# Kernel tuning notes

Measured on AMD Instinct MI355X. Metric: run time of the kernel, lower is better.

The kernel has to match this reference:

```python
import jax, jax.numpy as jnp
import numpy as np

B, N, SK, D, H = 4, 1024, 1024, 1024, 16
HD = D // H  # head_dim = 64


def _ln(x, w, b):
    # torch LayerNorm: biased variance, eps=1e-6
    m = x.mean(-1, keepdims=True)
    v = x.var(-1, keepdims=True)
    return (x - m) * jax.lax.rsqrt(v + 1e-6) * w + b


def setup_inputs() -> dict:
    key = jax.random.key(0)
    ks = jax.random.split(key, 16)
    def w(k, shape, s=0.02):
        return jax.random.normal(k, shape, jnp.float32) * s
    return dict(
        x=jax.random.normal(ks[0], (B, N, D), jnp.float32),
        k=jax.random.normal(ks[1], (N, H, SK, HD), jnp.float32),
        v=jax.random.normal(ks[2], (N, H, SK, HD), jnp.float32),
        qkv_w=w(ks[3], (D, 3 * D)), qkv_b=w(ks[4], (3 * D,)),
        sa_proj_w=w(ks[5], (D, D)), sa_proj_b=w(ks[6], (D,)),
        q_w=w(ks[7], (D, D)), q_b=w(ks[8], (D,)),
        ed_proj_w=w(ks[9], (D, D)), ed_proj_b=w(ks[10], (D,)),
        fc1_w=w(ks[11], (D, 4 * D)), fc1_b=w(ks[12], (4 * D,)),
        fc2_w=w(ks[13], (4 * D, D)), fc2_b=w(ks[14], (D,)),
        ln1_w=jnp.ones((D,)), ln1_b=jnp.zeros((D,)),
        ln2_w=jnp.ones((D,)), ln2_b=jnp.zeros((D,)),
        ln3_w=jnp.ones((D,)), ln3_b=jnp.zeros((D,)),
    )


def reference(x, k, v, qkv_w, qkv_b, sa_proj_w, sa_proj_b, q_w, q_b,
              ed_proj_w, ed_proj_b, fc1_w, fc1_b, fc2_w, fc2_b,
              ln1_w, ln1_b, ln2_w, ln2_b, ln3_w, ln3_b):
    scale = HD ** -0.5
    # ---- SelfAttention (faithful to the original, unusual einsums) ----
    qkv = (x @ qkv_w + qkv_b).reshape(B, N, 3, H, HD).transpose(2, 1, 3, 0, 4)
    q_s, k_s, v_s = qkv[0], qkv[1], qkv[2]  # each [N, H, B, HD]
    # no shared contraction index between k and q -> outer product of reductions
    dp = jnp.einsum('kabc,qdef->qabe', k_s, q_s) * scale  # [N, H, B, B]
    sc = jax.nn.softmax(dp, axis=-1)  # attn_p = 0.0 -> dropout is identity
    wa = jnp.einsum('qabc,kdef->bqaf', sc, v_s).reshape(B, N, D)
    sa = wa @ sa_proj_w + sa_proj_b
    h1 = _ln(sa + x, ln1_w, ln1_b)
    # ---- EncoderDecoderAttention ----
    qc = (h1 @ q_w + q_b).reshape(B, N, H, HD).transpose(1, 2, 0, 3)  # [N, H, B, HD]
    dp2 = jnp.einsum('abkd,abqd->abqk', k, qc) * scale  # [N, H, B, SK]
    sc2 = jax.nn.softmax(dp2, axis=-1)
    wa2 = jnp.einsum('abts,abse->tabe', sc2, v).reshape(B, N, D)
    ca = wa2 @ ed_proj_w + ed_proj_b
    h2 = _ln(ca + x, ln2_w, ln2_b)  # residual uses x (as in source)
    # ---- MLP (exact GELU, p=0 dropout) ----
    z = jax.nn.gelu(h2 @ fc1_w + fc1_b, approximate=False) @ fc2_w + fc2_b
    return _ln(z + h2, ln3_w, ln3_b)
```

## Files before the change

kernel.cpp:

```cpp
#include <hip/hip_runtime.h>
#include <hip/hip_bf16.h>
#include <math.h>

typedef __attribute__((ext_vector_type(8))) short bf16x8;
typedef __attribute__((ext_vector_type(4))) float f32x4;

__device__ __forceinline__ void gll16(const void* g, const void* l) {
  __builtin_amdgcn_global_load_lds((__attribute__((address_space(1))) void*)g,
                                   (__attribute__((address_space(3))) void*)l, 16, 0, 0);
}

__device__ __forceinline__ unsigned short bf16bits(float f) {
  __hip_bfloat16 h = __float2bfloat16(f);
  return *reinterpret_cast<unsigned short*>(&h);
}

__global__ __launch_bounds__(256) void k_transpose_bf16(
    const float* __restrict__ W, __hip_bfloat16* __restrict__ WT, int R, int C)
{
  __shared__ float t[32][33];
  const int c0 = blockIdx.x << 5, r0 = blockIdx.y << 5;
  const int tx = threadIdx.x & 31, ty = threadIdx.x >> 5;
#pragma unroll
  for (int i = 0; i < 32; i += 8)
    t[ty + i][tx] = W[(size_t)(r0 + ty + i) * C + c0 + tx];
  __syncthreads();
#pragma unroll
  for (int i = 0; i < 32; i += 8)
    WT[(size_t)(c0 + ty + i) * R + r0 + tx] = __float2bfloat16(t[tx][ty + i]);
}

__global__ __launch_bounds__(256) void k_colsum_part(const float* __restrict__ x, float* __restrict__ part) {
  const int d = blockIdx.x * 256 + threadIdx.x;
  const int r0 = blockIdx.y * 128;
  float acc = 0.f;
  for (int r = 0; r < 128; ++r) acc += x[(size_t)(r0 + r) * 1024 + d];
  part[blockIdx.y * 1024 + d] = acc;
}
__global__ __launch_bounds__(256) void k_colsum_fin(const float* __restrict__ part, float* __restrict__ Xsum) {
  const int d = blockIdx.x * 256 + threadIdx.x;
  float acc = 0.f;
  for (int y = 0; y < 32; ++y) acc += part[y * 1024 + d];
  Xsum[d] = acc;
}

__global__ __launch_bounds__(256) void k_matvec_t(const float* __restrict__ Xsum,
                                                  const float* __restrict__ qkv_w,
                                                  float* __restrict__ tmpt) {
  __shared__ float red[8][32];
  const int j = blockIdx.x * 32 + (threadIdx.x & 31);
  const int rg = threadIdx.x >> 5;
  float acc = 0.f;
  for (int r = rg; r < 1024; r += 8)
    acc += Xsum[r] * qkv_w[(size_t)r * 3072 + 2048 + j];
  red[rg][threadIdx.x & 31] = acc;
  __syncthreads();
  if (threadIdx.x < 32) {
    float s = 0.f;
    for (int gq = 0; gq < 8; ++gq) s += red[gq][threadIdx.x];
    tmpt[blockIdx.x * 32 + threadIdx.x] = s;
  }
}

__global__ void k_vsum(const float* __restrict__ tmpt, const float* __restrict__ qkv_b,
                       float* __restrict__ Vsum) {
  const int f = threadIdx.x;
  float acc = 0.f;
  for (int h = 0; h < 16; ++h)
    acc += tmpt[h * 64 + f] + 4096.0f * qkv_b[2048 + h * 64 + f];
  Vsum[f] = acc;
}

__global__ __launch_bounds__(256) void k_matvec_sa(const float* __restrict__ Vsum,
                                                   const float* __restrict__ saw,
                                                   const float* __restrict__ sab,
                                                   float* __restrict__ sarow) {
  __shared__ float red[8][32];
  const int j = blockIdx.x * 32 + (threadIdx.x & 31);
  const int rg = threadIdx.x >> 5;
  float acc = 0.f;
  for (int r = rg; r < 1024; r += 8)
    acc += Vsum[r & 63] * saw[(size_t)r * 1024 + j];
  red[rg][threadIdx.x & 31] = acc;
  __syncthreads();
  if (threadIdx.x < 32) {
    float s = 0.f;
    for (int gq = 0; gq < 8; ++gq) s += red[gq][threadIdx.x];
    sarow[blockIdx.x * 32 + threadIdx.x] = s + sab[blockIdx.x * 32 + threadIdx.x];
  }
}

__global__ __launch_bounds__(256) void k_ln(
    const float* __restrict__ a, const float* __restrict__ b,
    const float* __restrict__ rowadd, const float* __restrict__ w,
    const float* __restrict__ bias, float* __restrict__ outF,
    __hip_bfloat16* __restrict__ outB)
{
  const size_t base = (size_t)blockIdx.x * 1024;
  const int d4 = threadIdx.x << 2;
  float4 t = *(const float4*)(a + base + d4);
  if (b) { const float4 u = *(const float4*)(b + base + d4);
           t.x += u.x; t.y += u.y; t.z += u.z; t.w += u.w; }
  if (rowadd) { const float4 u = *(const float4*)(rowadd + d4);
                t.x += u.x; t.y += u.y; t.z += u.z; t.w += u.w; }
  float s1 = t.x + t.y + t.z + t.w;
  float s2 = t.x * t.x + t.y * t.y + t.z * t.z + t.w * t.w;
#pragma unroll
  for (int o = 32; o; o >>= 1) { s1 += __shfl_xor(s1, o); s2 += __shfl_xor(s2, o); }
  __shared__ float r1[4], r2[4];
  const int wv = threadIdx.x >> 6;
  if ((threadIdx.x & 63) == 0) { r1[wv] = s1; r2[wv] = s2; }
  __syncthreads();
  s1 = r1[0] + r1[1] + r1[2] + r1[3];
  s2 = r2[0] + r2[1] + r2[2] + r2[3];
  const float mean = s1 * (1.0f / 1024.0f);
  const float var = s2 * (1.0f / 1024.0f) - mean * mean;
  const float inv = rsqrtf(var + 1e-6f);
  const float4 w4 = *(const float4*)(w + d4);
  const float4 b4 = *(const float4*)(bias + d4);
  const float y0 = (t.x - mean) * inv * w4.x + b4.x;
  const float y1 = (t.y - mean) * inv * w4.y + b4.y;
  const float y2 = (t.z - mean) * inv * w4.z + b4.z;
  const float y3 = (t.w - mean) * inv * w4.w + b4.w;
  if (outF) *(float4*)(outF + base + d4) = make_float4(y0, y1, y2, y3);
  if (outB) {
    ushort4 u4; u4.x = bf16bits(y0); u4.y = bf16bits(y1); u4.z = bf16bits(y2); u4.w = bf16bits(y3);
    *(ushort4*)(outB + base + d4) = u4;
  }
}

template<int GELU, int OUTBF>
__global__ __launch_bounds__(256) void k_gemm_bt(
    const __hip_bfloat16* __restrict__ A, const __hip_bfloat16* __restrict__ BT,
    const float* __restrict__ bias, float* __restrict__ outF,
    __hip_bfloat16* __restrict__ outB, int M, int N, int K)
{
  __shared__ __align__(16) __hip_bfloat16 As[128 * 32];
  __shared__ __align__(16) __hip_bfloat16 Bs[128 * 32];
  const int tid = threadIdx.x;
  const int wave = tid >> 6, lane = tid & 63;
  const int m0 = blockIdx.y << 7, n0 = blockIdx.x << 7;
  const int wr = wave >> 1, wc = wave & 1;
  const int fr = lane & 15, fq = lane >> 4;
  f32x4 acc[4][4] = {};
  const int srow = (lane >> 2);
  const int scol = (lane & 3) * 8;
  for (int k0 = 0; k0 < K; k0 += 32) {
#pragma unroll
    for (int i = 0; i < 2; ++i) {
      const int chunk = wave * 2 + i;
      const int row = (chunk << 4) + srow;
      gll16(A + (size_t)(m0 + row) * K + k0 + scol, As + (chunk << 9));
      gll16(BT + (size_t)(n0 + row) * K + k0 + scol, Bs + (chunk << 9));
    }
    __syncthreads();
    bf16x8 af[4], bfr[4];
#pragma unroll
    for (int m = 0; m < 4; ++m)
      af[m] = *(const bf16x8*)(As + ((wr << 6) + (m << 4) + fr) * 32 + (fq << 3));
#pragma unroll
    for (int nn = 0; nn < 4; ++nn)
      bfr[nn] = *(const bf16x8*)(Bs + ((wc << 6) + (nn << 4) + fr) * 32 + (fq << 3));
#pragma unroll
    for (int m = 0; m < 4; ++m)
#pragma unroll
      for (int nn = 0; nn < 4; ++nn)
        acc[m][nn] = __builtin_amdgcn_mfma_f32_16x16x32_bf16(af[m], bfr[nn], acc[m][nn], 0, 0, 0);
    __syncthreads();
  }
#pragma unroll
  for (int m = 0; m < 4; ++m) {
#pragma unroll
    for (int nn = 0; nn < 4; ++nn) {
      const int col = n0 + (wc << 6) + (nn << 4) + fr;
      const float bv = bias[col];
#pragma unroll
      for (int j = 0; j < 4; ++j) {
        const int row = m0 + (wr << 6) + (m << 4) + (fq << 2) + j;
        float vv = acc[m][nn][j] + bv;
        if (GELU) vv = 0.5f * vv * (1.0f + erff(vv * 0.70710678118654752f));
        if (OUTBF) outB[(size_t)row * N + col] = __float2bfloat16(vv);
        else       outF[(size_t)row * N + col] = vv;
      }
    }
  }
}

__global__ __launch_bounds__(256) void k_attn(
    const float* __restrict__ kk, const float* __restrict__ vvg,
    const float* __restrict__ qc, __hip_bfloat16* __restrict__ wa2b)
{
  __shared__ __align__(16) float tile[2][64 * 64];
  __shared__ float p[4 * 1024];
  __shared__ __align__(16) float ql[4 * 64];
  __shared__ float denom[4];
  const int tid = threadIdx.x;
  const int wave = tid >> 6, lane = tid & 63;
  const int n = blockIdx.x >> 4, h = blockIdx.x & 15;
  const size_t kvbase = (size_t)(n * 16 + h) * (1024 * 64);

  ql[tid] = qc[((size_t)wave * 1024 + n) * 1024 + h * 64 + lane] * 0.125f;

  auto STAGE = [&](const float* __restrict__ src, int bi, int s0) {
#pragma unroll
    for (int i = 0; i < 4; ++i) {
      const int chunk = (wave << 2) + i;
      const int rl = (chunk << 2) + (lane >> 4);
      const int slot = (lane & 15) ^ (rl & 15);
      gll16(src + kvbase + (size_t)(s0 + rl) * 64 + (slot << 2), tile[bi] + (chunk << 8));
    }
  };

  STAGE(kk, 0, 0);
  __syncthreads();

  float4 qv[16];
#pragma unroll
  for (int i = 0; i < 16; ++i) qv[i] = *(const float4*)(ql + wave * 64 + (i << 2));

  const int sx = lane & 15;
  for (int t = 0; t < 16; ++t) {
    if (t < 15) STAGE(kk, (t + 1) & 1, (t + 1) << 6);
    else        STAGE(vvg, 0, 0);
    const float* tl = tile[t & 1];
    float a0 = 0.f;
#pragma unroll
    for (int d4 = 0; d4 < 16; ++d4) {
      const float4 kv = *(const float4*)(tl + lane * 64 + ((d4 ^ sx) << 2));
      const float4 qa = qv[d4];
      a0 += kv.x * qa.x + kv.y * qa.y + kv.z * qa.z + kv.w * qa.w;
    }
    p[wave * 1024 + (t << 6) + lane] = a0;
    __syncthreads();
  }

  {
    float mx = -1e30f;
#pragma unroll
    for (int j = 0; j < 16; ++j) mx = fmaxf(mx, p[wave * 1024 + (j << 6) + lane]);
#pragma unroll
    for (int o = 32; o; o >>= 1) mx = fmaxf(mx, __shfl_xor(mx, o));
    float sum = 0.f;
#pragma unroll
    for (int j = 0; j < 16; ++j) {
      const float e = __expf(p[wave * 1024 + (j << 6) + lane] - mx);
      p[wave * 1024 + (j << 6) + lane] = e;
      sum += e;
    }
#pragma unroll
    for (int o = 32; o; o >>= 1) sum += __shfl_xor(sum, o);
    if (lane == 0) denom[wave] = sum;
  }
  __syncthreads();

  const int sg = lane >> 4, e4 = lane & 15;
  float4 acc4 = make_float4(0.f, 0.f, 0.f, 0.f);
  for (int t = 0; t < 16; ++t) {
    if (t < 15) STAGE(vvg, (t + 1) & 1, (t + 1) << 6);
    const float* tl = tile[t & 1];
    const float* prow = p + wave * 1024 + (t << 6);
#pragma unroll
    for (int so = 0; so < 16; ++so) {
      const int s = (so << 2) + sg;
      const float pw = prow[s];
      const float4 vv = *(const float4*)(tl + s * 64 + ((e4 ^ (s & 15)) << 2));
      acc4.x += pw * vv.x; acc4.y += pw * vv.y; acc4.z += pw * vv.z; acc4.w += pw * vv.w;
    }
    __syncthreads();
  }
#pragma unroll
  for (int o = 16; o <= 32; o <<= 1) {
    acc4.x += __shfl_xor(acc4.x, o); acc4.y += __shfl_xor(acc4.y, o);
    acc4.z += __shfl_xor(acc4.z, o); acc4.w += __shfl_xor(acc4.w, o);
  }
  if (sg == 0) {
    const float inv = 1.0f / denom[wave];
    ushort4 u4;
    u4.x = bf16bits(acc4.x * inv); u4.y = bf16bits(acc4.y * inv);
    u4.z = bf16bits(acc4.z * inv); u4.w = bf16bits(acc4.w * inv);
    *(ushort4*)(wa2b + ((size_t)wave * 1024 + n) * 1024 + h * 64 + (e4 << 2)) = u4;
  }
}

extern "C" void kernel_launch(void* const* d_in, const int* in_sizes, int n_in,
                              void* d_out, int out_size, void* d_ws, size_t ws_size,
                              hipStream_t stream)
{
  (void)in_sizes; (void)n_in; (void)out_size; (void)ws_size;
  const float* x     = (const float*)d_in[0];
  const float* kin   = (const float*)d_in[1];
  const float* vin   = (const float*)d_in[2];
  const float* qkv_w = (const float*)d_in[3];
  const float* qkv_b = (const float*)d_in[4];
  const float* sa_w  = (const float*)d_in[5];
  const float* sa_b  = (const float*)d_in[6];
  const float* q_w   = (const float*)d_in[7];
  const float* q_b   = (const float*)d_in[8];
  const float* ed_w  = (const float*)d_in[9];
  const float* ed_b  = (const float*)d_in[10];
  const float* fc1_w = (const float*)d_in[11];
  const float* fc1_b = (const float*)d_in[12];
  const float* fc2_w = (const float*)d_in[13];
  const float* fc2_b = (const float*)d_in[14];
  const float* ln1_w = (const float*)d_in[15];
  const float* ln1_b = (const float*)d_in[16];
  const float* ln2_w = (const float*)d_in[17];
  const float* ln2_b = (const float*)d_in[18];
  const float* ln3_w = (const float*)d_in[19];
  const float* ln3_b = (const float*)d_in[20];
  float* out = (float*)d_out;

  char* ws = (char*)d_ws;
  constexpr size_t MB = 1024ull * 1024ull;
  float* part  = (float*)(ws + 0);
  float* Xsum  = (float*)(ws + 128 * 1024);
  float* tmpt  = (float*)(ws + 128 * 1024 + 4096);
  float* Vsum  = (float*)(ws + 128 * 1024 + 8192);
  float* sarow = (float*)(ws + 128 * 1024 + 12288);
  float*          qc   = (float*)(ws + 1 * MB);
  __hip_bfloat16* h1b  = (__hip_bfloat16*)(ws + 17 * MB);
  float*          ca   = (float*)(ws + 25 * MB);
  float*          h2   = (float*)(ws + 41 * MB);
  __hip_bfloat16* h2b  = (__hip_bfloat16*)(ws + 57 * MB);
  __hip_bfloat16* g    = (__hip_bfloat16*)(ws + 65 * MB);
  __hip_bfloat16* qwT  = (__hip_bfloat16*)(ws + 97 * MB);
  __hip_bfloat16* edwT = (__hip_bfloat16*)(ws + 99 * MB);
  __hip_bfloat16* f1wT = (__hip_bfloat16*)(ws + 101 * MB);
  __hip_bfloat16* f2wT = (__hip_bfloat16*)(ws + 109 * MB);
  float* z = qc;
  __hip_bfloat16* wa2b = h1b;

  k_transpose_bf16<<<dim3(32, 32), 256, 0, stream>>>(q_w, qwT, 1024, 1024);
  k_transpose_bf16<<<dim3(32, 32), 256, 0, stream>>>(ed_w, edwT, 1024, 1024);
  k_transpose_bf16<<<dim3(128, 32), 256, 0, stream>>>(fc1_w, f1wT, 1024, 4096);
  k_transpose_bf16<<<dim3(32, 128), 256, 0, stream>>>(fc2_w, f2wT, 4096, 1024);
  k_colsum_part<<<dim3(4, 32), 256, 0, stream>>>(x, part);
  k_colsum_fin<<<dim3(4), 256, 0, stream>>>(part, Xsum);
  k_matvec_t<<<dim3(32), 256, 0, stream>>>(Xsum, qkv_w, tmpt);
  k_vsum<<<dim3(1), 64, 0, stream>>>(tmpt, qkv_b, Vsum);
  k_matvec_sa<<<dim3(32), 256, 0, stream>>>(Vsum, sa_w, sa_b, sarow);
  k_ln<<<dim3(4096), 256, 0, stream>>>(x, nullptr, sarow, ln1_w, ln1_b, nullptr, h1b);
  k_gemm_bt<0, 0><<<dim3(8, 32), 256, 0, stream>>>(h1b, qwT, q_b, qc, nullptr, 4096, 1024, 1024);
  k_attn<<<dim3(16384), 256, 0, stream>>>(kin, vin, qc, wa2b);
  k_gemm_bt<0, 0><<<dim3(8, 32), 256, 0, stream>>>(wa2b, edwT, ed_b, ca, nullptr, 4096, 1024, 1024);
  k_ln<<<dim3(4096), 256, 0, stream>>>(ca, x, nullptr, ln2_w, ln2_b, h2, h2b);
  k_gemm_bt<1, 1><<<dim3(32, 32), 256, 0, stream>>>(h2b, f1wT, fc1_b, nullptr, g, 4096, 4096, 1024);
  k_gemm_bt<0, 0><<<dim3(8, 32), 256, 0, stream>>>(g, f2wT, fc2_b, z, nullptr, 4096, 1024, 4096);
  k_ln<<<dim3(4096), 256, 0, stream>>>(z, h2, nullptr, ln3_w, ln3_b, out, nullptr);
}
```

Before: 1.830 ms.

## Split-K the N=1024 GEMMs, merge transposes, and fold tiny reduction kernels

The three 4096x1024-output GEMMs now run with a two-way split along K through gridDim.z. Each half writes its own fp32 partial buffer, and the consumers (the attention q load and the LayerNorm kernels) add the two partials instead of a separate reduction pass. This doubles the block count from 256 to 512 to fill more CUs, at the cost of extra partial-buffer traffic. The four weight transposes are merged into one launch, and the colsum-finish and vsum kernels are folded into the matvec kernels to cut launch overhead.

```diff
diff --git a/kernel.cpp b/kernel.cpp
--- a/kernel.cpp
+++ b/kernel.cpp
@@ -15,11 +15,20 @@
   return *reinterpret_cast<unsigned short*>(&h);
 }
 
-__global__ __launch_bounds__(256) void k_transpose_bf16(
-    const float* __restrict__ W, __hip_bfloat16* __restrict__ WT, int R, int C)
+__global__ __launch_bounds__(256) void k_transpose4(
+    const float* __restrict__ W0, __hip_bfloat16* __restrict__ T0,
+    const float* __restrict__ W1, __hip_bfloat16* __restrict__ T1,
+    const float* __restrict__ W2, __hip_bfloat16* __restrict__ T2,
+    const float* __restrict__ W3, __hip_bfloat16* __restrict__ T3)
 {
   __shared__ float t[32][33];
-  const int c0 = blockIdx.x << 5, r0 = blockIdx.y << 5;
+  int b = blockIdx.x;
+  const float* W; __hip_bfloat16* T; int R, C, bx, by;
+  if (b < 1024)      { W = W0; T = T0; R = 1024; C = 1024; bx = b & 31;  by = b >> 5; }
+  else if (b < 2048) { b -= 1024; W = W1; T = T1; R = 1024; C = 1024; bx = b & 31;  by = b >> 5; }
+  else if (b < 6144) { b -= 2048; W = W2; T = T2; R = 1024; C = 4096; bx = b & 127; by = b >> 7; }
+  else               { b -= 6144; W = W3; T = T3; R = 4096; C = 1024; bx = b & 31;  by = b >> 5; }
+  const int c0 = bx << 5, r0 = by << 5;
   const int tx = threadIdx.x & 31, ty = threadIdx.x >> 5;
 #pragma unroll
   for (int i = 0; i < 32; i += 8)
@@ -27,7 +36,7 @@
   __syncthreads();
 #pragma unroll
   for (int i = 0; i < 32; i += 8)
-    WT[(size_t)(c0 + ty + i) * R + r0 + tx] = __float2bfloat16(t[tx][ty + i]);
+    T[(size_t)(c0 + ty + i) * R + r0 + tx] = __float2bfloat16(t[tx][ty + i]);
 }
 
 __global__ __launch_bounds__(256) void k_colsum_part(const float* __restrict__ x, float* __restrict__ part) {
@@ -37,22 +46,25 @@
   for (int r = 0; r < 128; ++r) acc += x[(size_t)(r0 + r) * 1024 + d];
   part[blockIdx.y * 1024 + d] = acc;
 }
-__global__ __launch_bounds__(256) void k_colsum_fin(const float* __restrict__ part, float* __restrict__ Xsum) {
-  const int d = blockIdx.x * 256 + threadIdx.x;
-  float acc = 0.f;
-  for (int y = 0; y < 32; ++y) acc += part[y * 1024 + d];
-  Xsum[d] = acc;
-}
-
-__global__ __launch_bounds__(256) void k_matvec_t(const float* __restrict__ Xsum,
+
+__global__ __launch_bounds__(256) void k_matvec_t(const float* __restrict__ part,
                                                   const float* __restrict__ qkv_w,
                                                   float* __restrict__ tmpt) {
+  __shared__ float xs[1024];
   __shared__ float red[8][32];
+#pragma unroll
+  for (int jj = 0; jj < 4; ++jj) {
+    const int d = threadIdx.x + (jj << 8);
+    float a = 0.f;
+    for (int y = 0; y < 32; ++y) a += part[y * 1024 + d];
+    xs[d] = a;
+  }
+  __syncthreads();
   const int j = blockIdx.x * 32 + (threadIdx.x & 31);
   const int rg = threadIdx.x >> 5;
   float acc = 0.f;
   for (int r = rg; r < 1024; r += 8)
-    acc += Xsum[r] * qkv_w[(size_t)r * 3072 + 2048 + j];
+    acc += xs[r] * qkv_w[(size_t)r * 3072 + 2048 + j];
   red[rg][threadIdx.x & 31] = acc;
   __syncthreads();
   if (threadIdx.x < 32) {
@@ -62,25 +74,25 @@
   }
 }
 
-__global__ void k_vsum(const float* __restrict__ tmpt, const float* __restrict__ qkv_b,
-                       float* __restrict__ Vsum) {
-  const int f = threadIdx.x;
-  float acc = 0.f;
-  for (int h = 0; h < 16; ++h)
-    acc += tmpt[h * 64 + f] + 4096.0f * qkv_b[2048 + h * 64 + f];
-  Vsum[f] = acc;
-}
-
-__global__ __launch_bounds__(256) void k_matvec_sa(const float* __restrict__ Vsum,
+__global__ __launch_bounds__(256) void k_matvec_sa(const float* __restrict__ tmpt,
+                                                   const float* __restrict__ qkv_b,
                                                    const float* __restrict__ saw,
                                                    const float* __restrict__ sab,
                                                    float* __restrict__ sarow) {
+  __shared__ float vs[64];
   __shared__ float red[8][32];
+  if (threadIdx.x < 64) {
+    float a = 0.f;
+    for (int h = 0; h < 16; ++h)
+      a += tmpt[h * 64 + threadIdx.x] + 4096.0f * qkv_b[2048 + h * 64 + threadIdx.x];
+    vs[threadIdx.x] = a;
+  }
+  __syncthreads();
   const int j = blockIdx.x * 32 + (threadIdx.x & 31);
   const int rg = threadIdx.x >> 5;
   float acc = 0.f;
   for (int r = rg; r < 1024; r += 8)
-    acc += Vsum[r & 63] * saw[(size_t)r * 1024 + j];
+    acc += vs[r & 63] * saw[(size_t)r * 1024 + j];
   red[rg][threadIdx.x & 31] = acc;
   __syncthreads();
   if (threadIdx.x < 32) {
@@ -91,7 +103,7 @@
 }
 
 __global__ __launch_bounds__(256) void k_ln(
-    const float* __restrict__ a, const float* __restrict__ b,
+    const float* __restrict__ a, const float* __restrict__ b, const float* __restrict__ c,
     const float* __restrict__ rowadd, const float* __restrict__ w,
     const float* __restrict__ bias, float* __restrict__ outF,
     __hip_bfloat16* __restrict__ outB)
@@ -100,6 +112,8 @@
   const int d4 = threadIdx.x << 2;
   float4 t = *(const float4*)(a + base + d4);
   if (b) { const float4 u = *(const float4*)(b + base + d4);
+           t.x += u.x; t.y += u.y; t.z += u.z; t.w += u.w; }
+  if (c) { const float4 u = *(const float4*)(c + base + d4);
            t.x += u.x; t.y += u.y; t.z += u.z; t.w += u.w; }
   if (rowadd) { const float4 u = *(const float4*)(rowadd + d4);
                 t.x += u.x; t.y += u.y; t.z += u.z; t.w += u.w; }
@@ -132,7 +146,7 @@
 template<int GELU, int OUTBF>
 __global__ __launch_bounds__(256) void k_gemm_bt(
     const __hip_bfloat16* __restrict__ A, const __hip_bfloat16* __restrict__ BT,
-    const float* __restrict__ bias, float* __restrict__ outF,
+    const float* __restrict__ bias, float* __restrict__ outF, float* __restrict__ outF2,
     __hip_bfloat16* __restrict__ outB, int M, int N, int K)
 {
   __shared__ __align__(16) __hip_bfloat16 As[128 * 32];
@@ -140,12 +154,16 @@
   const int tid = threadIdx.x;
   const int wave = tid >> 6, lane = tid & 63;
   const int m0 = blockIdx.y << 7, n0 = blockIdx.x << 7;
+  const int kl = K / gridDim.z;
+  const int ks = blockIdx.z * kl;
+  float* outP = blockIdx.z ? outF2 : outF;
+  const bool doBias = (blockIdx.z == 0);
   const int wr = wave >> 1, wc = wave & 1;
   const int fr = lane & 15, fq = lane >> 4;
   f32x4 acc[4][4] = {};
   const int srow = (lane >> 2);
   const int scol = (lane & 3) * 8;
-  for (int k0 = 0; k0 < K; k0 += 32) {
+  for (int k0 = ks; k0 < ks + kl; k0 += 32) {
 #pragma unroll
     for (int i = 0; i < 2; ++i) {
       const int chunk = wave * 2 + i;
@@ -173,14 +191,14 @@
 #pragma unroll
     for (int nn = 0; nn < 4; ++nn) {
       const int col = n0 + (wc << 6) + (nn << 4) + fr;
-      const float bv = bias[col];
+      const float bv = doBias ? bias[col] : 0.f;
 #pragma unroll
       for (int j = 0; j < 4; ++j) {
         const int row = m0 + (wr << 6) + (m << 4) + (fq << 2) + j;
         float vv = acc[m][nn][j] + bv;
         if (GELU) vv = 0.5f * vv * (1.0f + erff(vv * 0.70710678118654752f));
         if (OUTBF) outB[(size_t)row * N + col] = __float2bfloat16(vv);
-        else       outF[(size_t)row * N + col] = vv;
+        else       outP[(size_t)row * N + col] = vv;
       }
     }
   }
@@ -188,7 +206,8 @@
 
 __global__ __launch_bounds__(256) void k_attn(
     const float* __restrict__ kk, const float* __restrict__ vvg,
-    const float* __restrict__ qc, __hip_bfloat16* __restrict__ wa2b)
+    const float* __restrict__ qc1, const float* __restrict__ qc2,
+    __hip_bfloat16* __restrict__ wa2b)
 {
   __shared__ __align__(16) float tile[2][64 * 64];
   __shared__ float p[4 * 1024];
@@ -199,7 +218,10 @@
   const int n = blockIdx.x >> 4, h = blockIdx.x & 15;
   const size_t kvbase = (size_t)(n * 16 + h) * (1024 * 64);
 
-  ql[tid] = qc[((size_t)wave * 1024 + n) * 1024 + h * 64 + lane] * 0.125f;
+  {
+    const size_t qidx = ((size_t)wave * 1024 + n) * 1024 + h * 64 + lane;
+    ql[tid] = (qc1[qidx] + qc2[qidx]) * 0.125f;
+  }
 
   auto STAGE = [&](const float* __restrict__ src, int bi, int s0) {
 #pragma unroll
@@ -313,13 +335,11 @@
   char* ws = (char*)d_ws;
   constexpr size_t MB = 1024ull * 1024ull;
   float* part  = (float*)(ws + 0);
-  float* Xsum  = (float*)(ws + 128 * 1024);
-  float* tmpt  = (float*)(ws + 128 * 1024 + 4096);
-  float* Vsum  = (float*)(ws + 128 * 1024 + 8192);
-  float* sarow = (float*)(ws + 128 * 1024 + 12288);
-  float*          qc   = (float*)(ws + 1 * MB);
-  __hip_bfloat16* h1b  = (__hip_bfloat16*)(ws + 17 * MB);
-  float*          ca   = (float*)(ws + 25 * MB);
+  float* tmpt  = (float*)(ws + 192 * 1024);
+  float* sarow = (float*)(ws + 256 * 1024);
+  float* bufA  = (float*)(ws + 1 * MB);
+  float* bufB  = (float*)(ws + 17 * MB);
+  __hip_bfloat16* h1b  = (__hip_bfloat16*)(ws + 33 * MB);
   float*          h2   = (float*)(ws + 41 * MB);
   __hip_bfloat16* h2b  = (__hip_bfloat16*)(ws + 57 * MB);
   __hip_bfloat16* g    = (__hip_bfloat16*)(ws + 65 * MB);
@@ -327,24 +347,18 @@
   __hip_bfloat16* edwT = (__hip_bfloat16*)(ws + 99 * MB);
   __hip_bfloat16* f1wT = (__hip_bfloat16*)(ws + 101 * MB);
   __hip_bfloat16* f2wT = (__hip_bfloat16*)(ws + 109 * MB);
-  float* z = qc;
   __hip_bfloat16* wa2b = h1b;
 
-  k_transpose_bf16<<<dim3(32, 32), 256, 0, stream>>>(q_w, qwT, 1024, 1024);
-  k_transpose_bf16<<<dim3(32, 32), 256, 0, stream>>>(ed_w, edwT, 1024, 1024);
-  k_transpose_bf16<<<dim3(128, 32), 256, 0, stream>>>(fc1_w, f1wT, 1024, 4096);
-  k_transpose_bf16<<<dim3(32, 128), 256, 0, stream>>>(fc2_w, f2wT, 4096, 1024);
+  k_transpose4<<<dim3(10240), 256, 0, stream>>>(q_w, qwT, ed_w, edwT, fc1_w, f1wT, fc2_w, f2wT);
   k_colsum_part<<<dim3(4, 32), 256, 0, stream>>>(x, part);
-  k_colsum_fin<<<dim3(4), 256, 0, stream>>>(part, Xsum);
-  k_matvec_t<<<dim3(32), 256, 0, stream>>>(Xsum, qkv_w, tmpt);
-  k_vsum<<<dim3(1), 64, 0, stream>>>(tmpt, qkv_b, Vsum);
-  k_matvec_sa<<<dim3(32), 256, 0, stream>>>(Vsum, sa_w, sa_b, sarow);
-  k_ln<<<dim3(4096), 256, 0, stream>>>(x, nullptr, sarow, ln1_w, ln1_b, nullptr, h1b);
-  k_gemm_bt<0, 0><<<dim3(8, 32), 256, 0, stream>>>(h1b, qwT, q_b, qc, nullptr, 4096, 1024, 1024);
-  k_attn<<<dim3(16384), 256, 0, stream>>>(kin, vin, qc, wa2b);
-  k_gemm_bt<0, 0><<<dim3(8, 32), 256, 0, stream>>>(wa2b, edwT, ed_b, ca, nullptr, 4096, 1024, 1024);
-  k_ln<<<dim3(4096), 256, 0, stream>>>(ca, x, nullptr, ln2_w, ln2_b, h2, h2b);
-  k_gemm_bt<1, 1><<<dim3(32, 32), 256, 0, stream>>>(h2b, f1wT, fc1_b, nullptr, g, 4096, 4096, 1024);
-  k_gemm_bt<0, 0><<<dim3(8, 32), 256, 0, stream>>>(g, f2wT, fc2_b, z, nullptr, 4096, 1024, 4096);
-  k_ln<<<dim3(4096), 256, 0, stream>>>(z, h2, nullptr, ln3_w, ln3_b, out, nullptr);
-}
+  k_matvec_t<<<dim3(32), 256, 0, stream>>>(part, qkv_w, tmpt);
+  k_matvec_sa<<<dim3(32), 256, 0, stream>>>(tmpt, qkv_b, sa_w, sa_b, sarow);
+  k_ln<<<dim3(4096), 256, 0, stream>>>(x, nullptr, nullptr, sarow, ln1_w, ln1_b, nullptr, h1b);
+  k_gemm_bt<0, 0><<<dim3(8, 32, 2), 256, 0, stream>>>(h1b, qwT, q_b, bufA, bufB, nullptr, 4096, 1024, 1024);
+  k_attn<<<dim3(16384), 256, 0, stream>>>(kin, vin, bufA, bufB, wa2b);
+  k_gemm_bt<0, 0><<<dim3(8, 32, 2), 256, 0, stream>>>(wa2b, edwT, ed_b, bufA, bufB, nullptr, 4096, 1024, 1024);
+  k_ln<<<dim3(4096), 256, 0, stream>>>(bufA, bufB, x, nullptr, ln2_w, ln2_b, h2, h2b);
+  k_gemm_bt<1, 1><<<dim3(32, 32), 256, 0, stream>>>(h2b, f1wT, fc1_b, nullptr, nullptr, g, 4096, 4096, 1024);
+  k_gemm_bt<0, 0><<<dim3(8, 32, 2), 256, 0, stream>>>(g, f2wT, fc2_b, bufA, bufB, nullptr, 4096, 1024, 4096);
+  k_ln<<<dim3(4096), 256, 0, stream>>>(bufA, bufB, h2, nullptr, ln3_w, ln3_b, out, nullptr);
+}
```

Result: faster. 1.768 ms (-3.4%).
